# Kernel optimization log

Hardware: AMD Instinct MI355X
Metric: run time of the kernel (lower is better)

## Reference

```python
import jax, jax.numpy as jnp
import numpy as np

BLOCK_SIZE = 128


def setup_inputs() -> dict:
    key = jax.random.key(0)
    k1, k2, k3, k4 = jax.random.split(key, 4)
    B, T, C, H = 1024, 128, 1024, 64
    x = jax.random.normal(k1, (B, T, C), dtype=jnp.float32)
    # torch Linear(n_embed, head_size, bias=False): y = x @ W.T, W: [H, C].
    # Store as [C, H] for direct matmul (same math).
    scale = 1.0 / np.sqrt(C)
    Wk = jax.random.normal(k2, (C, H), dtype=jnp.float32) * scale
    Wq = jax.random.normal(k3, (C, H), dtype=jnp.float32) * scale
    Wv = jax.random.normal(k4, (C, H), dtype=jnp.float32) * scale
    return {"x": x, "Wk": Wk, "Wq": Wq, "Wv": Wv}


def reference(x, Wk, Wq, Wv):
    # Naive single-head causal attention, NO 1/sqrt(d) scaling (faithful to source).
    B, T, C = x.shape
    k = jnp.einsum('btc,ch->bth', x, Wk)  # [B,T,H]
    q = jnp.einsum('btc,ch->bth', x, Wq)  # [B,T,H]
    v = jnp.einsum('btc,ch->bth', x, Wv)  # [B,T,H]
    wei = jnp.einsum('bth,bsh->bts', q, k)  # [B,T,T] full score matrix
    causal = jnp.tril(jnp.ones((T, T), dtype=bool))
    wei = jnp.where(causal, wei, -jnp.inf)
    wei = jax.nn.softmax(wei, axis=-1)
    # dropout is identity in eval/reference mode
    out = jnp.einsum('bts,bsh->bth', wei, v)  # [B,T,H]
    return out
```

## Files before the change

kernel.cpp:

```cpp
#include <hip/hip_runtime.h>
#include <hip/hip_bf16.h>

typedef _Float16 half2_t __attribute__((ext_vector_type(2)));
typedef _Float16 half4_t __attribute__((ext_vector_type(4)));
typedef _Float16 half8_t __attribute__((ext_vector_type(8)));
typedef float    f32x4   __attribute__((ext_vector_type(4)));

static __device__ __forceinline__ half2_t pk2(float a, float b) {
#if __has_builtin(__builtin_amdgcn_cvt_pkrtz)
    auto r = __builtin_amdgcn_cvt_pkrtz(a, b);
    half2_t h; h[0] = (_Float16)r[0]; h[1] = (_Float16)r[1]; return h;
#else
    half2_t h; h[0] = (_Float16)a; h[1] = (_Float16)b; return h;
#endif
}

#if __has_builtin(__builtin_amdgcn_fdot2)
#define FDOT2(a, b, c) __builtin_amdgcn_fdot2((a), (b), (c), false)
#else
#define FDOT2(a, b, c) fmaf((float)(a)[0], (float)(b)[0], fmaf((float)(a)[1], (float)(b)[1], (c)))
#endif

__global__ __launch_bounds__(256) void cast_wT(const float* __restrict__ Wk,
                                               const float* __restrict__ Wq,
                                               const float* __restrict__ Wv,
                                               _Float16* __restrict__ wT) {
    int idx = blockIdx.x * 256 + threadIdx.x;
    int c = idx & 1023, n = idx >> 10;
    float v;
    if (n < 64)       v = Wk[c * 64 + n];
    else if (n < 128) v = Wq[c * 64 + (n - 64)];
    else              v = Wv[c * 64 + (n - 128)];
    wT[idx] = (_Float16)v;
}

#define LDA 40
#define LDB 40

__global__ __launch_bounds__(256, 3) void qkv_gemm(const float* __restrict__ x,
                                                   const _Float16* __restrict__ wT,
                                                   float* __restrict__ qkv) {
    __shared__ __align__(16) _Float16 As[128 * LDA];
    __shared__ __align__(16) _Float16 Bt[192 * LDB];

    const int tid  = threadIdx.x;
    const int m0   = blockIdx.x * 128;
    const int wave = tid >> 6;
    const int lane = tid & 63;
    const int wm   = wave * 32;
    const int lrow = lane & 15;
    const int lq   = lane >> 4;

    f32x4 acc[2][12] = {};

    const int arow = tid >> 3;
    const int acol = (tid & 7) * 4;
    const int brow = tid >> 2;
    const int bcol = (tid & 3) * 8;

    const float*    xg = x  + (size_t)(m0 + arow) * 1024 + acol;
    const _Float16* wg = wT + (size_t)brow * 1024 + bcol;

    for (int kb = 0; kb < 1024; kb += 32) {
        #pragma unroll
        for (int p = 0; p < 4; ++p) {
            float4 a = *(const float4*)(xg + (size_t)p * 32 * 1024 + kb);
            half2_t h0 = pk2(a.x, a.y), h1 = pk2(a.z, a.w);
            half4_t hv = {h0[0], h0[1], h1[0], h1[1]};
            *(half4_t*)&As[(arow + p * 32) * LDA + acol] = hv;
        }
        #pragma unroll
        for (int p = 0; p < 3; ++p) {
            half8_t bv = *(const half8_t*)(wg + (size_t)p * 64 * 1024 + kb);
            *(half8_t*)&Bt[(brow + p * 64) * LDB + bcol] = bv;
        }
        __syncthreads();

        half8_t aF0 = *(const half8_t*)&As[(wm + lrow) * LDA + lq * 8];
        half8_t aF1 = *(const half8_t*)&As[(wm + 16 + lrow) * LDA + lq * 8];
        #pragma unroll
        for (int nt = 0; nt < 12; ++nt) {
            half8_t bF = *(const half8_t*)&Bt[(nt * 16 + lrow) * LDB + lq * 8];
            acc[0][nt] = __builtin_amdgcn_mfma_f32_16x16x32_f16(aF0, bF, acc[0][nt], 0, 0, 0);
            acc[1][nt] = __builtin_amdgcn_mfma_f32_16x16x32_f16(aF1, bF, acc[1][nt], 0, 0, 0);
        }
        __syncthreads();
    }

    #pragma unroll
    for (int mt = 0; mt < 2; ++mt)
        #pragma unroll
        for (int nt = 0; nt < 12; ++nt)
            #pragma unroll
            for (int r = 0; r < 4; ++r) {
                int row = m0 + wm + mt * 16 + lq * 4 + r;
                int col = nt * 16 + lrow;
                qkv[(size_t)row * 192 + col] = acc[mt][nt][r];
            }
}

__global__ __launch_bounds__(256) void attn(const float* __restrict__ qkv,
                                            float* __restrict__ out) {
    __shared__ __align__(16) _Float16 ks[128 * 72];
    __shared__ __align__(16) _Float16 vT[64 * 136];
    __shared__ _Float16 ps16[4][128];

    const int b = blockIdx.x, t = threadIdx.x;
    const size_t base = (size_t)b * 128;

    {
        int j = t >> 1, h0 = (t & 1) * 32;
        const float4* krow = (const float4*)(qkv + (base + j) * 192 + h0);
        const float4* vrow = (const float4*)(qkv + (base + j) * 192 + 128 + h0);
        #pragma unroll
        for (int i = 0; i < 8; ++i) {
            float4 kv = krow[i];
            half2_t a = pk2(kv.x, kv.y), c = pk2(kv.z, kv.w);
            half4_t hv = {a[0], a[1], c[0], c[1]};
            *(half4_t*)&ks[j * 72 + h0 + i * 4] = hv;
            float4 vv = vrow[i];
            vT[(h0 + i * 4 + 0) * 136 + j] = (_Float16)vv.x;
            vT[(h0 + i * 4 + 1) * 136 + j] = (_Float16)vv.y;
            vT[(h0 + i * 4 + 2) * 136 + j] = (_Float16)vv.z;
            vT[(h0 + i * 4 + 3) * 136 + j] = (_Float16)vv.w;
        }
    }
    __syncthreads();

    const int wave = t >> 6, lane = t & 63;
    const half8_t* k0p = (const half8_t*)&ks[lane * 72];
    const half8_t* k1p = (const half8_t*)&ks[(64 + lane) * 72];
    const half8_t* vp  = (const half8_t*)&vT[lane * 136];

    for (int rr = 0; rr < 32; ++rr) {
        const int row = rr * 4 + wave;
        const float4* qg = (const float4*)(qkv + (base + row) * 192 + 64);

        float s0 = 0.f, s1 = -INFINITY;
        {
            float s0a = 0.f, s0b = 0.f;
            if (row >= 64) {
                float s1a = 0.f, s1b = 0.f;
                #pragma unroll
                for (int i = 0; i < 8; ++i) {
                    float4 qA = qg[2 * i], qB = qg[2 * i + 1];
                    half2_t q0 = pk2(qA.x, qA.y), q1 = pk2(qA.z, qA.w);
                    half2_t q2 = pk2(qB.x, qB.y), q3 = pk2(qB.z, qB.w);
                    half8_t ka = k0p[i], kb = k1p[i];
                    half2_t c0 = {ka[0], ka[1]}, c1 = {ka[2], ka[3]}, c2 = {ka[4], ka[5]}, c3 = {ka[6], ka[7]};
                    half2_t d0 = {kb[0], kb[1]}, d1 = {kb[2], kb[3]}, d2 = {kb[4], kb[5]}, d3 = {kb[6], kb[7]};
                    s0a = FDOT2(q0, c0, s0a); s0b = FDOT2(q1, c1, s0b);
                    s0a = FDOT2(q2, c2, s0a); s0b = FDOT2(q3, c3, s0b);
                    s1a = FDOT2(q0, d0, s1a); s1b = FDOT2(q1, d1, s1b);
                    s1a = FDOT2(q2, d2, s1a); s1b = FDOT2(q3, d3, s1b);
                }
                s0 = s0a + s0b;
                s1 = (64 + lane <= row) ? (s1a + s1b) : -INFINITY;
            } else {
                #pragma unroll
                for (int i = 0; i < 8; ++i) {
                    float4 qA = qg[2 * i], qB = qg[2 * i + 1];
                    half2_t q0 = pk2(qA.x, qA.y), q1 = pk2(qA.z, qA.w);
                    half2_t q2 = pk2(qB.x, qB.y), q3 = pk2(qB.z, qB.w);
                    half8_t ka = k0p[i];
                    half2_t c0 = {ka[0], ka[1]}, c1 = {ka[2], ka[3]}, c2 = {ka[4], ka[5]}, c3 = {ka[6], ka[7]};
                    s0a = FDOT2(q0, c0, s0a); s0b = FDOT2(q1, c1, s0b);
                    s0a = FDOT2(q2, c2, s0a); s0b = FDOT2(q3, c3, s0b);
                }
                s0 = (lane <= row) ? (s0a + s0b) : -INFINITY;
            }
        }
        float m = fmaxf(s0, s1);
        #pragma unroll
        for (int d = 1; d < 64; d <<= 1) m = fmaxf(m, __shfl_xor(m, d, 64));
        float p0 = __expf(s0 - m), p1 = __expf(s1 - m);
        float l = p0 + p1;
        #pragma unroll
        for (int d = 1; d < 64; d <<= 1) l += __shfl_xor(l, d, 64);
        float inv = 1.f / l;
        ps16[wave][lane]      = (_Float16)(p0 * inv);
        ps16[wave][64 + lane] = (_Float16)(p1 * inv);

        const int nj = row + 1;
        float o0 = 0.f, o1 = 0.f, o2 = 0.f, o3 = 0.f;
        const int n8 = nj >> 3;
        for (int i = 0; i < n8; ++i) {
            half8_t pv = *(const half8_t*)&ps16[wave][i * 8];
            half8_t vv = vp[i];
            half2_t pa = {pv[0], pv[1]}, pb = {pv[2], pv[3]}, pc = {pv[4], pv[5]}, pd = {pv[6], pv[7]};
            half2_t va = {vv[0], vv[1]}, vb = {vv[2], vv[3]}, vc = {vv[4], vv[5]}, vd = {vv[6], vv[7]};
            o0 = FDOT2(pa, va, o0); o1 = FDOT2(pb, vb, o1);
            o2 = FDOT2(pc, vc, o2); o3 = FDOT2(pd, vd, o3);
        }
        for (int j = n8 * 8; j < nj; ++j)
            o0 = fmaf((float)ps16[wave][j], (float)vT[lane * 136 + j], o0);

        out[(base + row) * 64 + lane] = (o0 + o1) + (o2 + o3);
    }
}

extern "C" void kernel_launch(void* const* d_in, const int* in_sizes, int n_in,
                              void* d_out, int out_size, void* d_ws, size_t ws_size,
                              hipStream_t stream) {
    const float* x  = (const float*)d_in[0];
    const float* Wk = (const float*)d_in[1];
    const float* Wq = (const float*)d_in[2];
    const float* Wv = (const float*)d_in[3];
    float* out = (float*)d_out;

    _Float16* wT  = (_Float16*)d_ws;
    float*    qkv = (float*)((char*)d_ws + (size_t)192 * 1024 * 2);

    cast_wT<<<768, 256, 0, stream>>>(Wk, Wq, Wv, wT);
    qkv_gemm<<<1024, 256, 0, stream>>>(x, wT, qkv);
    attn<<<1024, 256, 0, stream>>>(qkv, out);
}
```

Baseline: 862.6 us.

## Fuse QKV projection GEMM and causal attention into one kernel

Merges the QKV GEMM and the attention kernel into a single kernel per batch element. The GEMM results are written straight into shared memory as fp16 K, Q and transposed V, reusing the GEMM staging buffers, so the global fp32 qkv round trip and the second launch go away. In exchange, shared memory per block grows to about 54KB and the occupancy hint drops from 3 to 2 blocks, which may reduce latency hiding in the GEMM phase.

```diff
diff --git a/kernel.cpp b/kernel.cpp
--- a/kernel.cpp
+++ b/kernel.cpp
@@ -37,14 +37,20 @@
 #define LDA 40
 #define LDB 40
 
-__global__ __launch_bounds__(256, 3) void qkv_gemm(const float* __restrict__ x,
-                                                   const _Float16* __restrict__ wT,
-                                                   float* __restrict__ qkv) {
-    __shared__ __align__(16) _Float16 As[128 * LDA];
-    __shared__ __align__(16) _Float16 Bt[192 * LDB];
+__global__ __launch_bounds__(256, 2) void fused_head(const float* __restrict__ x,
+                                                     const _Float16* __restrict__ wT,
+                                                     float* __restrict__ out) {
+    __shared__ __align__(16) char smem[55296];
+    _Float16* As = (_Float16*)smem;
+    _Float16* Bt = (_Float16*)(smem + 10240);
+    _Float16* ks = (_Float16*)smem;
+    _Float16* qs = (_Float16*)(smem + 18432);
+    _Float16* vT = (_Float16*)(smem + 36864);
+    _Float16* ps = (_Float16*)(smem + 54272);
 
     const int tid  = threadIdx.x;
-    const int m0   = blockIdx.x * 128;
+    const int b    = blockIdx.x;
+    const int m0   = b * 128;
     const int wave = tid >> 6;
     const int lane = tid & 63;
     const int wm   = wave * 32;
@@ -93,48 +99,23 @@
         for (int nt = 0; nt < 12; ++nt)
             #pragma unroll
             for (int r = 0; r < 4; ++r) {
-                int row = m0 + wm + mt * 16 + lq * 4 + r;
+                int row = wm + mt * 16 + lq * 4 + r;
                 int col = nt * 16 + lrow;
-                qkv[(size_t)row * 192 + col] = acc[mt][nt][r];
+                float v = acc[mt][nt][r];
+                if (nt < 4)      ks[row * 72 + col] = (_Float16)v;
+                else if (nt < 8) qs[row * 72 + (col - 64)] = (_Float16)v;
+                else             vT[(col - 128) * 136 + row] = (_Float16)v;
             }
-}
-
-__global__ __launch_bounds__(256) void attn(const float* __restrict__ qkv,
-                                            float* __restrict__ out) {
-    __shared__ __align__(16) _Float16 ks[128 * 72];
-    __shared__ __align__(16) _Float16 vT[64 * 136];
-    __shared__ _Float16 ps16[4][128];
-
-    const int b = blockIdx.x, t = threadIdx.x;
-    const size_t base = (size_t)b * 128;
-
-    {
-        int j = t >> 1, h0 = (t & 1) * 32;
-        const float4* krow = (const float4*)(qkv + (base + j) * 192 + h0);
-        const float4* vrow = (const float4*)(qkv + (base + j) * 192 + 128 + h0);
-        #pragma unroll
-        for (int i = 0; i < 8; ++i) {
-            float4 kv = krow[i];
-            half2_t a = pk2(kv.x, kv.y), c = pk2(kv.z, kv.w);
-            half4_t hv = {a[0], a[1], c[0], c[1]};
-            *(half4_t*)&ks[j * 72 + h0 + i * 4] = hv;
-            float4 vv = vrow[i];
-            vT[(h0 + i * 4 + 0) * 136 + j] = (_Float16)vv.x;
-            vT[(h0 + i * 4 + 1) * 136 + j] = (_Float16)vv.y;
-            vT[(h0 + i * 4 + 2) * 136 + j] = (_Float16)vv.z;
-            vT[(h0 + i * 4 + 3) * 136 + j] = (_Float16)vv.w;
-        }
-    }
     __syncthreads();
 
-    const int wave = t >> 6, lane = t & 63;
     const half8_t* k0p = (const half8_t*)&ks[lane * 72];
     const half8_t* k1p = (const half8_t*)&ks[(64 + lane) * 72];
     const half8_t* vp  = (const half8_t*)&vT[lane * 136];
+    _Float16* psw = ps + wave * 128;
 
     for (int rr = 0; rr < 32; ++rr) {
         const int row = rr * 4 + wave;
-        const float4* qg = (const float4*)(qkv + (base + row) * 192 + 64);
+        const half8_t* qp = (const half8_t*)&qs[row * 72];
 
         float s0 = 0.f, s1 = -INFINITY;
         {
@@ -143,12 +124,12 @@
                 float s1a = 0.f, s1b = 0.f;
                 #pragma unroll
                 for (int i = 0; i < 8; ++i) {
-                    float4 qA = qg[2 * i], qB = qg[2 * i + 1];
-                    half2_t q0 = pk2(qA.x, qA.y), q1 = pk2(qA.z, qA.w);
-                    half2_t q2 = pk2(qB.x, qB.y), q3 = pk2(qB.z, qB.w);
-                    half8_t ka = k0p[i], kb = k1p[i];
+                    half8_t qv = qp[i];
+                    half2_t q0 = {qv[0], qv[1]}, q1 = {qv[2], qv[3]};
+                    half2_t q2 = {qv[4], qv[5]}, q3 = {qv[6], qv[7]};
+                    half8_t ka = k0p[i], kb2 = k1p[i];
                     half2_t c0 = {ka[0], ka[1]}, c1 = {ka[2], ka[3]}, c2 = {ka[4], ka[5]}, c3 = {ka[6], ka[7]};
-                    half2_t d0 = {kb[0], kb[1]}, d1 = {kb[2], kb[3]}, d2 = {kb[4], kb[5]}, d3 = {kb[6], kb[7]};
+                    half2_t d0 = {kb2[0], kb2[1]}, d1 = {kb2[2], kb2[3]}, d2 = {kb2[4], kb2[5]}, d3 = {kb2[6], kb2[7]};
                     s0a = FDOT2(q0, c0, s0a); s0b = FDOT2(q1, c1, s0b);
                     s0a = FDOT2(q2, c2, s0a); s0b = FDOT2(q3, c3, s0b);
                     s1a = FDOT2(q0, d0, s1a); s1b = FDOT2(q1, d1, s1b);
@@ -159,9 +140,9 @@
             } else {
                 #pragma unroll
                 for (int i = 0; i < 8; ++i) {
-                    float4 qA = qg[2 * i], qB = qg[2 * i + 1];
-                    half2_t q0 = pk2(qA.x, qA.y), q1 = pk2(qA.z, qA.w);
-                    half2_t q2 = pk2(qB.x, qB.y), q3 = pk2(qB.z, qB.w);
+                    half8_t qv = qp[i];
+                    half2_t q0 = {qv[0], qv[1]}, q1 = {qv[2], qv[3]};
+                    half2_t q2 = {qv[4], qv[5]}, q3 = {qv[6], qv[7]};
                     half8_t ka = k0p[i];
                     half2_t c0 = {ka[0], ka[1]}, c1 = {ka[2], ka[3]}, c2 = {ka[4], ka[5]}, c3 = {ka[6], ka[7]};
                     s0a = FDOT2(q0, c0, s0a); s0b = FDOT2(q1, c1, s0b);
@@ -178,14 +159,14 @@
         #pragma unroll
         for (int d = 1; d < 64; d <<= 1) l += __shfl_xor(l, d, 64);
         float inv = 1.f / l;
-        ps16[wave][lane]      = (_Float16)(p0 * inv);
-        ps16[wave][64 + lane] = (_Float16)(p1 * inv);
+        psw[lane]      = (_Float16)(p0 * inv);
+        psw[64 + lane] = (_Float16)(p1 * inv);
 
         const int nj = row + 1;
         float o0 = 0.f, o1 = 0.f, o2 = 0.f, o3 = 0.f;
         const int n8 = nj >> 3;
         for (int i = 0; i < n8; ++i) {
-            half8_t pv = *(const half8_t*)&ps16[wave][i * 8];
+            half8_t pv = *(const half8_t*)&psw[i * 8];
             half8_t vv = vp[i];
             half2_t pa = {pv[0], pv[1]}, pb = {pv[2], pv[3]}, pc = {pv[4], pv[5]}, pd = {pv[6], pv[7]};
             half2_t va = {vv[0], vv[1]}, vb = {vv[2], vv[3]}, vc = {vv[4], vv[5]}, vd = {vv[6], vv[7]};
@@ -193,9 +174,9 @@
             o2 = FDOT2(pc, vc, o2); o3 = FDOT2(pd, vd, o3);
         }
         for (int j = n8 * 8; j < nj; ++j)
-            o0 = fmaf((float)ps16[wave][j], (float)vT[lane * 136 + j], o0);
+            o0 = fmaf((float)psw[j], (float)vT[lane * 136 + j], o0);
 
-        out[(base + row) * 64 + lane] = (o0 + o1) + (o2 + o3);
+        out[((size_t)m0 + row) * 64 + lane] = (o0 + o1) + (o2 + o3);
     }
 }
 
@@ -208,10 +189,8 @@
     const float* Wv = (const float*)d_in[3];
     float* out = (float*)d_out;
 
-    _Float16* wT  = (_Float16*)d_ws;
-    float*    qkv = (float*)((char*)d_ws + (size_t)192 * 1024 * 2);
+    _Float16* wT = (_Float16*)d_ws;
 
     cast_wT<<<768, 256, 0, stream>>>(Wk, Wq, Wv, wT);
-    qkv_gemm<<<1024, 256, 0, stream>>>(x, wT, qkv);
-    attn<<<1024, 256, 0, stream>>>(qkv, out);
+    fused_head<<<1024, 256, 0, stream>>>(x, wT, out);
 }
```

Result: faster. 838.6 us (-2.8%).
